# Performance work log

Measured on AMD Instinct MI355X. Metric: run time of the kernel, lower is better.

## Reference

```python
import jax, jax.numpy as jnp
import numpy as np

B, T, C = 2, 1024, 2048
H, N = 32, 64
D_DECAY = 96; D_AAA = 96; D_MV = 64; D_GATE = 256
EPS_GN = 1e-5 * 64.0  # eps * head_size_divisor**2, divisor=8


def setup_inputs() -> dict:
    key = jax.random.key(0)
    ks = jax.random.split(key, 24)
    rn = lambda k, s, sc=1.0: jax.random.normal(k, s, jnp.float32) * sc
    ru = lambda k, s: jax.random.uniform(k, s, jnp.float32)
    sw = C ** -0.5
    return dict(
        x=rn(ks[0], (B, T, C)),
        v_first=rn(ks[1], (B, T, C)),
        shift_state=rn(ks[2], (B, C)),
        wkv_state=jnp.zeros((B, H, N, N), jnp.float32),
        x_r=ru(ks[3], (1, 1, C)), x_w=ru(ks[4], (1, 1, C)), x_k=ru(ks[5], (1, 1, C)),
        x_v=ru(ks[6], (1, 1, C)), x_a=ru(ks[7], (1, 1, C)), x_g=ru(ks[8], (1, 1, C)),
        w0=jnp.linspace(-7.0, -2.0, C, dtype=jnp.float32).reshape(1, 1, C) + 0.5,
        w1=rn(ks[9], (C, D_DECAY), sw), w2=rn(ks[10], (D_DECAY, C), 0.1 * D_DECAY ** -0.5),
        a0=jnp.zeros((1, 1, C), jnp.float32),
        a1=rn(ks[11], (C, D_AAA), sw), a2=rn(ks[12], (D_AAA, C), 0.1 * D_AAA ** -0.5),
        v0=jnp.ones((1, 1, C), jnp.float32),
        v1=rn(ks[13], (C, D_MV), sw), v2=rn(ks[14], (D_MV, C), 0.1 * D_MV ** -0.5),
        g1=rn(ks[15], (C, D_GATE), sw), g2=rn(ks[16], (D_GATE, C), 0.1 * D_GATE ** -0.5),
        k_k=0.85 * jnp.ones((1, 1, C), jnp.float32),
        k_a=jnp.ones((1, 1, C), jnp.float32),
        r_k=rn(ks[17], (H, N), 0.1),
        W_r=rn(ks[18], (C, C), sw), W_k=rn(ks[19], (C, C), sw),
        W_v=rn(ks[20], (C, C), sw), W_o=rn(ks[21], (C, C), sw),
        gn_w=jnp.ones((C,), jnp.float32), gn_b=jnp.zeros((C,), jnp.float32),
    )


def _forward(x, v_first, shift_state, wkv_state, x_r, x_w, x_k, x_v, x_a, x_g,
             w0, w1, w2, a0, a1, a2, v0, v1, v2, g1, g2, k_k, k_a, r_k,
             W_r, W_k, W_v, W_o, gn_w, gn_b):
    # token shift (ZeroPad2d((0,0,1,-1)) == prepend shift_state, drop last)
    xx = jnp.concatenate([shift_state[:, None, :], x[:, :-1]], axis=1) - x
    xr = x + xx * x_r; xw = x + xx * x_w; xk = x + xx * x_k
    xv = x + xx * x_v; xa = x + xx * x_a; xg = x + xx * x_g
    r = xr @ W_r.T
    w = -jax.nn.softplus(-(w0 + jnp.tanh(xw @ w1) @ w2)) - 0.5  # <= -0.5
    k = xk @ W_k.T
    v = xv @ W_v.T
    v = v + (v_first - v) * jax.nn.sigmoid(v0 + (xv @ v1) @ v2)  # layer_id != 0
    a = jax.nn.sigmoid(a0 + (xa @ a1) @ a2)
    g = jax.nn.sigmoid(xg @ g1) @ g2
    kk = (k * k_k).reshape(B, T, H, N)
    kk = kk / jnp.maximum(jnp.linalg.norm(kk, axis=-1, keepdims=True), 1e-12)  # F.normalize
    k = k * (1.0 + (a - 1.0) * k_a)
    # RWKV-7 recurrence: S_t = S * diag(exp(-exp(w))) + (S a) b^T + v k^T ; o_t = S r
    wdec = jnp.exp(-jnp.exp(w))                           # [B,T,C] in (0,1)
    tm = lambda z: z.reshape(B, T, H, N).transpose(1, 0, 2, 3)  # -> [T,B,H,N]
    xs = (tm(r), tm(wdec), tm(k), tm(v),
          -kk.transpose(1, 0, 2, 3),
          (kk * a.reshape(B, T, H, N)).transpose(1, 0, 2, 3))

    def step(S, ins):  # S: [B,H,N_v,N_k]
        rr, ww, kc, vv, aa, bb = ins
        Sa = jnp.einsum('bhvk,bhk->bhv', S, aa)
        S = S * ww[:, :, None, :] + Sa[..., None] * bb[:, :, None, :] + vv[..., None] * kc[:, :, None, :]
        return S, jnp.einsum('bhvk,bhk->bhv', S, rr)

    S_f, o = jax.lax.scan(step, wkv_state, xs)
    o = o.transpose(1, 0, 2, 3)                           # [B,T,H,N]
    # GroupNorm(H, C): per-(B*T) sample, normalize each head's N channels
    mu = o.mean(-1, keepdims=True)
    var = o.var(-1, keepdims=True)
    o = (o - mu) * jax.lax.rsqrt(var + EPS_GN) * gn_w.reshape(H, N) + gn_b.reshape(H, N)
    rh = r.reshape(B, T, H, N); kh = k.reshape(B, T, H, N); vh = v.reshape(B, T, H, N)
    o = o + (rh * kh * r_k).sum(-1, keepdims=True) * vh
    out = (o.reshape(B, T, C) * g) @ W_o.T
    return out, S_f


def reference(x, v_first, shift_state, wkv_state, x_r, x_w, x_k, x_v, x_a, x_g,
              w0, w1, w2, a0, a1, a2, v0, v1, v2, g1, g2, k_k, k_a, r_k,
              W_r, W_k, W_v, W_o, gn_w, gn_b):
    out, S_f = _forward(x, v_first, shift_state, wkv_state, x_r, x_w, x_k, x_v, x_a, x_g,
                        w0, w1, w2, a0, a1, a2, v0, v1, v2, g1, g2, k_k, k_a, r_k,
                        W_r, W_k, W_v, W_o, gn_w, gn_b)
    return (out, S_f)
```

## Files before the change

kernel.cpp:

```cpp
#include <hip/hip_runtime.h>
#include <stdint.h>

typedef __attribute__((ext_vector_type(4))) float f32x4;
typedef __attribute__((ext_vector_type(8))) __bf16 bf16x8;

#define DEVINL __device__ __forceinline__

constexpr int T_LEN = 1024;
constexpr int CDIM  = 2048;
constexpr int MROWS = 2048;
constexpr size_t MC = (size_t)MROWS * CDIM;

constexpr size_t SZ_BF  = MC * 2;
constexpr size_t SZ_F32 = MC * 4;
constexpr size_t oXr  = 0;
constexpr size_t oXw  = oXr + SZ_BF;
constexpr size_t oXk  = oXw + SZ_BF;
constexpr size_t oXv  = oXk + SZ_BF;
constexpr size_t oXa  = oXv + SZ_BF;
constexpr size_t oXg  = oXa + SZ_BF;
constexpr size_t oWr  = oXg + SZ_BF;
constexpr size_t oWk  = oWr + SZ_BF;
constexpr size_t oWv  = oWk + SZ_BF;
constexpr size_t oWo  = oWv + SZ_BF;
constexpr size_t oW1T = oWo + SZ_BF;
constexpr size_t oA1T = oW1T + 524288;
constexpr size_t oV1T = oA1T + 524288;
constexpr size_t oG1T = oV1T + 524288;
constexpr size_t oW2T = oG1T + 1048576;
constexpr size_t oA2T = oW2T + 524288;
constexpr size_t oV2T = oA2T + 524288;
constexpr size_t oG2T = oV2T + 524288;
constexpr size_t oHw  = oG2T + 1048576;
constexpr size_t oHa  = oHw + 524288;
constexpr size_t oHv  = oHa + 524288;
constexpr size_t oHg  = oHv + 524288;
constexpr size_t oR   = oHg + 1048576;
constexpr size_t oK   = oR  + SZ_F32;
constexpr size_t oV   = oK  + SZ_F32;
constexpr size_t oWW  = oV  + SZ_F32;
constexpr size_t oAA  = oWW + SZ_F32;
constexpr size_t oBB  = oAA + SZ_F32;
constexpr size_t oG   = oBB + SZ_F32;
constexpr size_t oO   = oG  + SZ_F32;
constexpr size_t oAout= oO  + SZ_F32;

DEVINL unsigned short f2bf(float f) {
  uint32_t u = __builtin_bit_cast(uint32_t, f);
  u += 0x7fffu + ((u >> 16) & 1u);
  return (unsigned short)(u >> 16);
}
DEVINL void st_bf4(unsigned short* p, f32x4 v) {
  ushort4 o;
  o.x = f2bf(v[0]); o.y = f2bf(v[1]); o.z = f2bf(v[2]); o.w = f2bf(v[3]);
  *(ushort4*)p = o;
}
DEVINL void gload16(const void* g, void* l) {
  __builtin_amdgcn_global_load_lds(
      (const __attribute__((address_space(1))) unsigned int*)g,
      (__attribute__((address_space(3))) unsigned int*)l, 16, 0, 0);
}

DEVINL float red8(float x) {
  int y = __builtin_amdgcn_update_dpp(0, __builtin_bit_cast(int, x),
                                      0x128, 0xF, 0xF, true);
  return x + __builtin_bit_cast(float, y);
}
#if __has_builtin(__builtin_amdgcn_permlane16_swap)
DEVINL float red16(float x, bool evenrow) {
  unsigned xi = __builtin_bit_cast(unsigned, x);
  auto r = __builtin_amdgcn_permlane16_swap(xi, xi, false, false);
  unsigned oth = evenrow ? (unsigned)r[1] : (unsigned)r[0];
  return x + __builtin_bit_cast(float, oth);
}
#else
DEVINL float red16(float x, bool) { return x + __shfl_xor(x, 16); }
#endif
#if __has_builtin(__builtin_amdgcn_permlane32_swap)
DEVINL float red32(float x, bool lowhalf) {
  unsigned xi = __builtin_bit_cast(unsigned, x);
  auto r = __builtin_amdgcn_permlane32_swap(xi, xi, false, false);
  unsigned oth = lowhalf ? (unsigned)r[1] : (unsigned)r[0];
  return x + __builtin_bit_cast(float, oth);
}
#else
DEVINL float red32(float x, bool) { return x + __shfl_xor(x, 32); }
#endif

struct Conv4 { const float* s0; const float* s1; const float* s2; const float* s3;
               unsigned short* d0; unsigned short* d1; unsigned short* d2; unsigned short* d3; };
__global__ void k_conv4(Conv4 c, int n4) {
  int i = blockIdx.x * 256 + threadIdx.x;
  if (i >= n4) return;
  const float* s = (blockIdx.y == 0) ? c.s0 : (blockIdx.y == 1) ? c.s1
                   : (blockIdx.y == 2) ? c.s2 : c.s3;
  unsigned short* d = (blockIdx.y == 0) ? c.d0 : (blockIdx.y == 1) ? c.d1
                      : (blockIdx.y == 2) ? c.d2 : c.d3;
  f32x4 v = *(const f32x4*)(s + (size_t)i * 4);
  st_bf4(d + (size_t)i * 4, v);
}

struct TpJobs {
  const float* src[8];
  unsigned short* dst[8];
  int sR[8]; int sC[8]; int dR[8]; int dC[8];
};
__global__ void k_tp8(TpJobs jt) {
  const int j = blockIdx.y;
  const int n = jt.dR[j] * jt.dC[j];
  int i = blockIdx.x * 256 + threadIdx.x;
  if (i >= n) return;
  const int dC = jt.dC[j], sR = jt.sR[j], sC = jt.sC[j];
  int r = i / dC, c = i - r * dC;
  float v = (r < sC && c < sR) ? jt.src[j][(size_t)c * sC + r] : 0.f;
  jt.dst[j][i] = f2bf(v);
}

__global__ void k_mix(const float* __restrict__ x, const float* __restrict__ shift,
                      const float* __restrict__ cr, const float* __restrict__ cw,
                      const float* __restrict__ ck, const float* __restrict__ cv,
                      const float* __restrict__ ca, const float* __restrict__ cg,
                      unsigned short* __restrict__ Xr, unsigned short* __restrict__ Xw,
                      unsigned short* __restrict__ Xk, unsigned short* __restrict__ Xv,
                      unsigned short* __restrict__ Xa, unsigned short* __restrict__ Xg) {
  int i = blockIdx.x * 256 + threadIdx.x;
  size_t e = (size_t)i * 4;
  int m = (int)(e >> 11);
  int c = (int)(e & 2047);
  int t = m & (T_LEN - 1);
  int b = m >> 10;
  f32x4 xc = *(const f32x4*)(x + e);
  f32x4 pv = (t == 0) ? *(const f32x4*)(shift + (size_t)b * CDIM + c)
                      : *(const f32x4*)(x + e - CDIM);
  f32x4 xx = pv - xc;
  st_bf4(Xr + e, xc + xx * (*(const f32x4*)(cr + c)));
  st_bf4(Xw + e, xc + xx * (*(const f32x4*)(cw + c)));
  st_bf4(Xk + e, xc + xx * (*(const f32x4*)(ck + c)));
  st_bf4(Xv + e, xc + xx * (*(const f32x4*)(cv + c)));
  st_bf4(Xa + e, xc + xx * (*(const f32x4*)(ca + c)));
  st_bf4(Xg + e, xc + xx * (*(const f32x4*)(cg + c)));
}

struct GemmJob { const unsigned short* A; const unsigned short* B; void* C; int epi; int ldc; int n; };
struct GemmBatch { GemmJob j[4]; };

__global__ __launch_bounds__(256) void k_gemm_nt(GemmBatch gb, int K) {
  const GemmJob jb = gb.j[blockIdx.z];
  const int colB = blockIdx.x * 128;
  if (colB >= jb.n) return;
  const int ldc = jb.ldc;
  __shared__ __align__(16) unsigned short As[128 * 32];
  __shared__ __align__(16) unsigned short Bs[128 * 32];
  const int tid  = threadIdx.x;
  const int lane = tid & 63;
  const int wv   = tid >> 6;
  const int wm = wv >> 1, wn = wv & 1;
  const int rowB = blockIdx.y * 128;
  const size_t rsb = (size_t)K * 2;
  const int c0 = wv, c1 = wv + 4;
  const char* Ag0 = (const char*)jb.A + (size_t)(rowB + c0 * 16 + (lane >> 2)) * rsb + (lane & 3) * 16;
  const char* Ag1 = (const char*)jb.A + (size_t)(rowB + c1 * 16 + (lane >> 2)) * rsb + (lane & 3) * 16;
  const char* Bg0 = (const char*)jb.B + (size_t)(colB + c0 * 16 + (lane >> 2)) * rsb + (lane & 3) * 16;
  const char* Bg1 = (const char*)jb.B + (size_t)(colB + c1 * 16 + (lane >> 2)) * rsb + (lane & 3) * 16;
  unsigned short* Al0 = As + c0 * 512;
  unsigned short* Al1 = As + c1 * 512;
  unsigned short* Bl0 = Bs + c0 * 512;
  unsigned short* Bl1 = Bs + c1 * 512;
  f32x4 acc[4][4];
#pragma unroll
  for (int mi = 0; mi < 4; ++mi)
#pragma unroll
    for (int ni = 0; ni < 4; ++ni) acc[mi][ni] = (f32x4){0.f, 0.f, 0.f, 0.f};
  const int KT = K >> 5;
  const int fr = lane & 15, fk = (lane >> 4) * 8;
  for (int kt = 0; kt < KT; ++kt) {
    __syncthreads();
    gload16(Ag0, Al0); gload16(Ag1, Al1);
    gload16(Bg0, Bl0); gload16(Bg1, Bl1);
    Ag0 += 64; Ag1 += 64; Bg0 += 64; Bg1 += 64;
    __syncthreads();
    bf16x8 af[4], bfv[4];
#pragma unroll
    for (int mi = 0; mi < 4; ++mi)
      af[mi] = *(const bf16x8*)&As[(wm * 64 + mi * 16 + fr) * 32 + fk];
#pragma unroll
    for (int ni = 0; ni < 4; ++ni)
      bfv[ni] = *(const bf16x8*)&Bs[(wn * 64 + ni * 16 + fr) * 32 + fk];
#pragma unroll
    for (int mi = 0; mi < 4; ++mi)
#pragma unroll
      for (int ni = 0; ni < 4; ++ni)
        acc[mi][ni] = __builtin_amdgcn_mfma_f32_16x16x32_bf16(af[mi], bfv[ni], acc[mi][ni], 0, 0, 0);
  }
  const int er = (lane >> 4) * 4, ec = lane & 15;
  if (jb.epi == 0) {
    float* Cf = (float*)jb.C;
#pragma unroll
    for (int mi = 0; mi < 4; ++mi)
#pragma unroll
      for (int ni = 0; ni < 4; ++ni) {
        int row0 = rowB + wm * 64 + mi * 16 + er;
        int col  = colB + wn * 64 + ni * 16 + ec;
#pragma unroll
        for (int j = 0; j < 4; ++j)
          Cf[(size_t)(row0 + j) * ldc + col] = acc[mi][ni][j];
      }
  } else {
    unsigned short* Cb = (unsigned short*)jb.C;
#pragma unroll
    for (int mi = 0; mi < 4; ++mi)
#pragma unroll
      for (int ni = 0; ni < 4; ++ni) {
        int row0 = rowB + wm * 64 + mi * 16 + er;
        int col  = colB + wn * 64 + ni * 16 + ec;
#pragma unroll
        for (int j = 0; j < 4; ++j) {
          float val = acc[mi][ni][j];
          if (jb.epi == 2) val = tanhf(val);
          else if (jb.epi == 3) val = 1.f / (1.f + __expf(-val));
          Cb[(size_t)(row0 + j) * ldc + col] = f2bf(val);
        }
      }
  }
}

__global__ __launch_bounds__(256) void k_post(
    float* __restrict__ Kb, float* __restrict__ Vb, float* __restrict__ Wb,
    float* __restrict__ Ab, float* __restrict__ Bb,
    const float* __restrict__ vf, const float* __restrict__ w0,
    const float* __restrict__ a0, const float* __restrict__ v0,
    const float* __restrict__ kkc, const float* __restrict__ kac) {
  int gw = blockIdx.x * 4 + (threadIdx.x >> 6);
  int lane = threadIdx.x & 63;
  int m = gw >> 5, h = gw & 31;
  int c = h * 64 + lane;
  size_t idx = (size_t)m * CDIM + c;
  float kraw = Kb[idx], vraw = Vb[idx], wlr = Wb[idx], alr = Ab[idx], vlr = Bb[idx];
  float z = w0[c] + wlr;
  float sg = 1.f / (1.f + __expf(-z));
  float wdec = __expf(-0.60653065971f * sg);
  float a = 1.f / (1.f + __expf(-(a0[c] + alr)));
  float vgate = 1.f / (1.f + __expf(-(v0[c] + vlr)));
  float v = vraw + (vf[idx] - vraw) * vgate;
  float kk = kraw * kkc[c];
  float s2 = kk * kk;
#pragma unroll
  for (int off = 32; off; off >>= 1) s2 += __shfl_xor(s2, off);
  float inv = 1.f / fmaxf(sqrtf(s2), 1e-12f);
  kk *= inv;
  float kn = kraw * (1.f + (a - 1.f) * kac[c]);
  Wb[idx] = wdec; Vb[idx] = v; Kb[idx] = kn; Ab[idx] = -kk; Bb[idx] = kk * a;
}

__global__ __launch_bounds__(64) void k_scan(
    const float* __restrict__ Rb, const float* __restrict__ Wb,
    const float* __restrict__ Kb, const float* __restrict__ Vb,
    const float* __restrict__ Ab, const float* __restrict__ Bb,
    const float* __restrict__ S0, float* __restrict__ Ob,
    float* __restrict__ Sf) {
  const int bid = blockIdx.x;
  const int bh = bid & 63, vo = bid >> 6;
  const int b = bh >> 5, h = bh & 31;
  const int lane = threadIdx.x;
  const int vr = lane & 7;
  const int kq = lane >> 3;
  const int gv = vo * 8 + vr;
  const int kk0 = kq * 8;
  const bool evr = ((lane >> 4) & 1) == 0;
  const bool lhf = lane < 32;
  __shared__ __align__(16) float stg[4][6][64];
  const size_t rowBase = (size_t)b * T_LEN * CDIM;
  const size_t colBase = (size_t)h * 64;
  const float* pR = Rb + rowBase + colBase + lane;
  const float* pW = Wb + rowBase + colBase + lane;
  const float* pK = Kb + rowBase + colBase + lane;
  const float* pV = Vb + rowBase + colBase + lane;
  const float* pA = Ab + rowBase + colBase + lane;
  const float* pB = Bb + rowBase + colBase + lane;
  float* Obp = Ob + rowBase + colBase + vo * 8 + lane;
  f32x4 s0, s1;
  {
    const float* sp = S0 + (((size_t)(b * 32 + h)) * 64 + gv) * 64 + kk0;
    s0 = *(const f32x4*)sp; s1 = *(const f32x4*)(sp + 4);
  }
  float gA[6], gB[6];
  {
    float h0[6], h1[6];
    h0[0] = pR[0]; h0[1] = pW[0]; h0[2] = pK[0]; h0[3] = pV[0]; h0[4] = pA[0]; h0[5] = pB[0];
    h1[0] = pR[CDIM]; h1[1] = pW[CDIM]; h1[2] = pK[CDIM]; h1[3] = pV[CDIM]; h1[4] = pA[CDIM]; h1[5] = pB[CDIM];
#pragma unroll
    for (int j = 0; j < 6; ++j) { stg[0][j][lane] = h0[j]; stg[1][j][lane] = h1[j]; }
    gA[0] = pR[2 * CDIM]; gA[1] = pW[2 * CDIM]; gA[2] = pK[2 * CDIM];
    gA[3] = pV[2 * CDIM]; gA[4] = pA[2 * CDIM]; gA[5] = pB[2 * CDIM];
    gB[0] = pR[3 * CDIM]; gB[1] = pW[3 * CDIM]; gB[2] = pK[3 * CDIM];
    gB[3] = pV[3 * CDIM]; gB[4] = pA[3 * CDIM]; gB[5] = pB[3 * CDIM];
  }
  f32x4 aR0, aR1, aW0, aW1, aK0, aK1, aA0, aA1, aB0, aB1; float aVV;
  f32x4 bR0, bR1, bW0, bW1, bK0, bK1, bA0, bA1, bB0, bB1; float bVV;
  aR0 = *(const f32x4*)&stg[0][0][kk0]; aR1 = *(const f32x4*)&stg[0][0][kk0 + 4];
  aW0 = *(const f32x4*)&stg[0][1][kk0]; aW1 = *(const f32x4*)&stg[0][1][kk0 + 4];
  aK0 = *(const f32x4*)&stg[0][2][kk0]; aK1 = *(const f32x4*)&stg[0][2][kk0 + 4];
  aA0 = *(const f32x4*)&stg[0][4][kk0]; aA1 = *(const f32x4*)&stg[0][4][kk0 + 4];
  aB0 = *(const f32x4*)&stg[0][5][kk0]; aB1 = *(const f32x4*)&stg[0][5][kk0 + 4];
  aVV = stg[0][3][gv];
  float pox = 0.f;
#define SCAN_STEP(T, G, SR0,SR1,SW0,SW1,SK0,SK1,SA0,SA1,SB0,SB1,SVV,           \
                  NR0,NR1,NW0,NW1,NK0,NK1,NA0,NA1,NB0,NB1,NVV, FIRST) do {     \
    f32x4 _sv = SA0 * s0 + SA1 * s1;                                           \
    float _sa = _sv[0] + _sv[1] + _sv[2] + _sv[3];                             \
    { const int _np = ((T) + 1) & 3;          \
      NR0 = *(const f32x4*)&stg[_np][0][kk0]; NR1 = *(const f32x4*)&stg[_np][0][kk0 + 4]; \
      NW0 = *(const f32x4*)&stg[_np][1][kk0]; NW1 = *(const f32x4*)&stg[_np][1][kk0 + 4]; \
      NK0 = *(const f32x4*)&stg[_np][2][kk0]; NK1 = *(const f32x4*)&stg[_np][2][kk0 + 4]; \
      NA0 = *(const f32x4*)&stg[_np][4][kk0]; NA1 = *(const f32x4*)&stg[_np][4][kk0 + 4]; \
      NB0 = *(const f32x4*)&stg[_np][5][kk0]; NB1 = *(const f32x4*)&stg[_np][5][kk0 + 4]; \
      NVV = stg[_np][3][gv]; }                                                 \
    float _po = pox;                                                           \
    _sa = red8(_sa);        _po = red8(_po);                                   \
    _sa = red16(_sa, evr);  _po = red16(_po, evr);                             \
    _sa = red32(_sa, lhf);  _po = red32(_po, lhf);                             \
    if (!(FIRST) && lane < 8) Obp[(size_t)((T) - 1) * CDIM] = _po;             \
    { const int _ws = ((T) + 2) & 3;                                           \
      stg[_ws][0][lane] = G[0]; stg[_ws][1][lane] = G[1];                      \
      stg[_ws][2][lane] = G[2]; stg[_ws][3][lane] = G[3];                      \
      stg[_ws][4][lane] = G[4]; stg[_ws][5][lane] = G[5];                      \
      const size_t _to = (size_t)(((T) + 4 < T_LEN) ? (T) + 4 : T_LEN - 1) * CDIM; \
      G[0] = pR[_to]; G[1] = pW[_to]; G[2] = pK[_to];                          \
      G[3] = pV[_to]; G[4] = pA[_to]; G[5] = pB[_to]; }                        \
    s0 = s0 * SW0 + _sa * SB0 + SVV * SK0;                                     \
    s1 = s1 * SW1 + _sa * SB1 + SVV * SK1;                                     \
    f32x4 _ov = s0 * SR0 + s1 * SR1;                                           \
    pox = _ov[0] + _ov[1] + _ov[2] + _ov[3];                                   \
  } while (0)
#define SCAN_STEP_I(...) SCAN_STEP(__VA_ARGS__)
#define ASET aR0,aR1,aW0,aW1,aK0,aK1,aA0,aA1,aB0,aB1,aVV
#define BSET bR0,bR1,bW0,bW1,bK0,bK1,bA0,bA1,bB0,bB1,bVV
  SCAN_STEP_I(0, gA, ASET, BSET, true);
  SCAN_STEP_I(1, gB, BSET, ASET, false);
  for (int t = 2; t < T_LEN; t += 2) {
    SCAN_STEP_I(t, gA, ASET, BSET, false);
    SCAN_STEP_I(t + 1, gB, BSET, ASET, false);
  }
#undef SCAN_STEP
#undef SCAN_STEP_I
#undef ASET
#undef BSET
  {
    float _po = pox;
    _po = red8(_po);
    _po = red16(_po, evr);
    _po = red32(_po, lhf);
    if (lane < 8) Obp[(size_t)(T_LEN - 1) * CDIM] = _po;
  }
  float* sfp = Sf + (((size_t)(b * 32 + h)) * 64 + gv) * 64 + kk0;
  *(f32x4*)sfp = s0; *(f32x4*)(sfp + 4) = s1;
}

__global__ __launch_bounds__(256) void k_gn(
    const float* __restrict__ Ob, const float* __restrict__ Rb,
    const float* __restrict__ Kb, const float* __restrict__ Vb,
    const float* __restrict__ Gb, const float* __restrict__ rk,
    const float* __restrict__ gw, const float* __restrict__ gb2,
    unsigned short* __restrict__ Aout) {
  int gwv = blockIdx.x * 4 + (threadIdx.x >> 6);
  int lane = threadIdx.x & 63;
  int m = gwv >> 5, h = gwv & 31;
  int c = h * 64 + lane;
  size_t idx = (size_t)m * CDIM + c;
  float o = Ob[idx], r = Rb[idx], k = Kb[idx], v = Vb[idx], g = Gb[idx];
  float t1 = o, t2 = o * o, t3 = r * k * rk[c];
#pragma unroll
  for (int off = 32; off; off >>= 1) {
    t1 += __shfl_xor(t1, off);
    t2 += __shfl_xor(t2, off);
    t3 += __shfl_xor(t3, off);
  }
  float mean = t1 * (1.f / 64.f);
  float var = t2 * (1.f / 64.f) - mean * mean;
  float og = (o - mean) * rsqrtf(var + 6.4e-4f) * gw[c] + gb2[c];
  og += t3 * v;
  Aout[idx] = f2bf(og * g);
}

extern "C" void kernel_launch(void* const* d_in, const int* in_sizes, int n_in,
                              void* d_out, int out_size, void* d_ws, size_t ws_size,
                              hipStream_t stream) {
  (void)in_sizes; (void)n_in; (void)out_size; (void)ws_size;
  const float* x      = (const float*)d_in[0];
  const float* vfirst = (const float*)d_in[1];
  const float* shift  = (const float*)d_in[2];
  const float* wkv0   = (const float*)d_in[3];
  const float* xr_c   = (const float*)d_in[4];
  const float* xw_c   = (const float*)d_in[5];
  const float* xk_c   = (const float*)d_in[6];
  const float* xv_c   = (const float*)d_in[7];
  const float* xa_c   = (const float*)d_in[8];
  const float* xg_c   = (const float*)d_in[9];
  const float* w0     = (const float*)d_in[10];
  const float* w1     = (const float*)d_in[11];
  const float* w2     = (const float*)d_in[12];
  const float* a0     = (const float*)d_in[13];
  const float* a1     = (const float*)d_in[14];
  const float* a2     = (const float*)d_in[15];
  const float* v0     = (const float*)d_in[16];
  const float* v1     = (const float*)d_in[17];
  const float* v2     = (const float*)d_in[18];
  const float* g1     = (const float*)d_in[19];
  const float* g2     = (const float*)d_in[20];
  const float* k_k    = (const float*)d_in[21];
  const float* k_a    = (const float*)d_in[22];
  const float* r_k    = (const float*)d_in[23];
  const float* W_r    = (const float*)d_in[24];
  const float* W_k    = (const float*)d_in[25];
  const float* W_v    = (const float*)d_in[26];
  const float* W_o    = (const float*)d_in[27];
  const float* gn_w   = (const float*)d_in[28];
  const float* gn_b   = (const float*)d_in[29];
  char* ws = (char*)d_ws;
  auto BF = [&](size_t o) { return (unsigned short*)(ws + o); };
  auto FP = [&](size_t o) { return (float*)(ws + o); };

  { Conv4 cb{W_r, W_k, W_v, W_o, BF(oWr), BF(oWk), BF(oWv), BF(oWo)};
    k_conv4<<<dim3(4096, 4), 256, 0, stream>>>(cb, 1048576); }
  { TpJobs jt{};
    jt.src[0] = w1; jt.dst[0] = BF(oW1T); jt.sR[0] = 2048; jt.sC[0] = 96;   jt.dR[0] = 128;  jt.dC[0] = 2048;
    jt.src[1] = a1; jt.dst[1] = BF(oA1T); jt.sR[1] = 2048; jt.sC[1] = 96;   jt.dR[1] = 128;  jt.dC[1] = 2048;
    jt.src[2] = v1; jt.dst[2] = BF(oV1T); jt.sR[2] = 2048; jt.sC[2] = 64;   jt.dR[2] = 128;  jt.dC[2] = 2048;
    jt.src[3] = g1; jt.dst[3] = BF(oG1T); jt.sR[3] = 2048; jt.sC[3] = 256;  jt.dR[3] = 256;  jt.dC[3] = 2048;
    jt.src[4] = w2; jt.dst[4] = BF(oW2T); jt.sR[4] = 96;   jt.sC[4] = 2048; jt.dR[4] = 2048; jt.dC[4] = 128;
    jt.src[5] = a2; jt.dst[5] = BF(oA2T); jt.sR[5] = 96;   jt.sC[5] = 2048; jt.dR[5] = 2048; jt.dC[5] = 128;
    jt.src[6] = v2; jt.dst[6] = BF(oV2T); jt.sR[6] = 64;   jt.sC[6] = 2048; jt.dR[6] = 2048; jt.dC[6] = 128;
    jt.src[7] = g2; jt.dst[7] = BF(oG2T); jt.sR[7] = 256;  jt.sC[7] = 2048; jt.dR[7] = 2048; jt.dC[7] = 256;
    k_tp8<<<dim3(2048, 8), 256, 0, stream>>>(jt); }
  k_mix<<<4096, 256, 0, stream>>>(x, shift, xr_c, xw_c, xk_c, xv_c, xa_c, xg_c,
                                  BF(oXr), BF(oXw), BF(oXk), BF(oXv), BF(oXa), BF(oXg));
  { GemmBatch gb{};
    gb.j[0] = {BF(oXr), BF(oWr), FP(oR), 0, 2048, 2048};
    gb.j[1] = {BF(oXk), BF(oWk), FP(oK), 0, 2048, 2048};
    gb.j[2] = {BF(oXv), BF(oWv), FP(oV), 0, 2048, 2048};
    k_gemm_nt<<<dim3(16, 16, 3), 256, 0, stream>>>(gb, 2048); }
  { GemmBatch gb{};
    gb.j[0] = {BF(oXw), BF(oW1T), BF(oHw), 2, 128, 128};
    gb.j[1] = {BF(oXa), BF(oA1T), BF(oHa), 1, 128, 128};
    gb.j[2] = {BF(oXv), BF(oV1T), BF(oHv), 1, 128, 128};
    gb.j[3] = {BF(oXg), BF(oG1T), BF(oHg), 3, 256, 256};
    k_gemm_nt<<<dim3(2, 16, 4), 256, 0, stream>>>(gb, 2048); }
  { GemmBatch gb{};
    gb.j[0] = {BF(oHw), BF(oW2T), FP(oWW), 0, 2048, 2048};
    gb.j[1] = {BF(oHa), BF(oA2T), FP(oAA), 0, 2048, 2048};
    gb.j[2] = {BF(oHv), BF(oV2T), FP(oBB), 0, 2048, 2048};
    k_gemm_nt<<<dim3(16, 16, 3), 256, 0, stream>>>(gb, 128); }
  { GemmBatch gb{};
    gb.j[0] = {BF(oHg), BF(oG2T), FP(oG), 0, 2048, 2048};
    k_gemm_nt<<<dim3(16, 16, 1), 256, 0, stream>>>(gb, 256); }
  k_post<<<16384, 256, 0, stream>>>(FP(oK), FP(oV), FP(oWW), FP(oAA), FP(oBB),
                                    vfirst, w0, a0, v0, k_k, k_a);
  k_scan<<<512, 64, 0, stream>>>(FP(oR), FP(oWW), FP(oK), FP(oV), FP(oAA), FP(oBB),
                                 wkv0, FP(oO), (float*)d_out + MC);
  k_gn<<<16384, 256, 0, stream>>>(FP(oO), FP(oR), FP(oK), FP(oV), FP(oG),
                                  r_k, gn_w, gn_b, BF(oAout));
  { GemmBatch gb{};
    gb.j[0] = {BF(oAout), BF(oWo), d_out, 0, 2048, 2048};
    k_gemm_nt<<<dim3(16, 16, 1), 256, 0, stream>>>(gb, 2048); }
}
```

Measured before the change: 587.1 us.

## Halve per-wave state rows in WKV scan and double scan grid

The recurrent scan kernel now gives each wave 4 value rows instead of 8, with each lane holding 4 state elements instead of 8. The grid doubles from 512 to 1024 single-wave blocks, so there are more independent waves per CU to hide the latency of the sequential per-step dependency chain. In exchange, every block still loads the full per-step r/w/k/v/a/b vectors, so global and LDS staging traffic doubles. The cross-lane reduction also gains an extra DPP rotate step, which lengthens each step's critical path.

```diff
diff --git a/kernel.cpp b/kernel.cpp
--- a/kernel.cpp
+++ b/kernel.cpp
@@ -61,9 +61,10 @@
       (__attribute__((address_space(3))) unsigned int*)l, 16, 0, 0);
 }
 
-DEVINL float red8(float x) {
+template <int CTL>
+DEVINL float redrot(float x) {
   int y = __builtin_amdgcn_update_dpp(0, __builtin_bit_cast(int, x),
-                                      0x128, 0xF, 0xF, true);
+                                      CTL, 0xF, 0xF, true);
   return x + __builtin_bit_cast(float, y);
 }
 #if __has_builtin(__builtin_amdgcn_permlane16_swap)
@@ -262,10 +263,10 @@
   const int bh = bid & 63, vo = bid >> 6;
   const int b = bh >> 5, h = bh & 31;
   const int lane = threadIdx.x;
-  const int vr = lane & 7;
-  const int kq = lane >> 3;
-  const int gv = vo * 8 + vr;
-  const int kk0 = kq * 8;
+  const int vr = lane & 3;
+  const int kq = lane >> 2;
+  const int gv = vo * 4 + vr;
+  const int kk0 = kq * 4;
   const bool evr = ((lane >> 4) & 1) == 0;
   const bool lhf = lane < 32;
   __shared__ __align__(16) float stg[4][6][64];
@@ -277,11 +278,11 @@
   const float* pV = Vb + rowBase + colBase + lane;
   const float* pA = Ab + rowBase + colBase + lane;
   const float* pB = Bb + rowBase + colBase + lane;
-  float* Obp = Ob + rowBase + colBase + vo * 8 + lane;
-  f32x4 s0, s1;
+  float* Obp = Ob + rowBase + colBase + vo * 4 + lane;
+  f32x4 s0;
   {
     const float* sp = S0 + (((size_t)(b * 32 + h)) * 64 + gv) * 64 + kk0;
-    s0 = *(const f32x4*)sp; s1 = *(const f32x4*)(sp + 4);
+    s0 = *(const f32x4*)sp;
   }
   float gA[6], gB[6];
   {
@@ -295,31 +296,31 @@
     gB[0] = pR[3 * CDIM]; gB[1] = pW[3 * CDIM]; gB[2] = pK[3 * CDIM];
     gB[3] = pV[3 * CDIM]; gB[4] = pA[3 * CDIM]; gB[5] = pB[3 * CDIM];
   }
-  f32x4 aR0, aR1, aW0, aW1, aK0, aK1, aA0, aA1, aB0, aB1; float aVV;
-  f32x4 bR0, bR1, bW0, bW1, bK0, bK1, bA0, bA1, bB0, bB1; float bVV;
-  aR0 = *(const f32x4*)&stg[0][0][kk0]; aR1 = *(const f32x4*)&stg[0][0][kk0 + 4];
-  aW0 = *(const f32x4*)&stg[0][1][kk0]; aW1 = *(const f32x4*)&stg[0][1][kk0 + 4];
-  aK0 = *(const f32x4*)&stg[0][2][kk0]; aK1 = *(const f32x4*)&stg[0][2][kk0 + 4];
-  aA0 = *(const f32x4*)&stg[0][4][kk0]; aA1 = *(const f32x4*)&stg[0][4][kk0 + 4];
-  aB0 = *(const f32x4*)&stg[0][5][kk0]; aB1 = *(const f32x4*)&stg[0][5][kk0 + 4];
+  f32x4 aR, aW, aK, aA, aB; float aVV;
+  f32x4 bR, bW, bK, bA, bB; float bVV;
+  aR = *(const f32x4*)&stg[0][0][kk0];
+  aW = *(const f32x4*)&stg[0][1][kk0];
+  aK = *(const f32x4*)&stg[0][2][kk0];
+  aA = *(const f32x4*)&stg[0][4][kk0];
+  aB = *(const f32x4*)&stg[0][5][kk0];
   aVV = stg[0][3][gv];
   float pox = 0.f;
-#define SCAN_STEP(T, G, SR0,SR1,SW0,SW1,SK0,SK1,SA0,SA1,SB0,SB1,SVV,           \
-                  NR0,NR1,NW0,NW1,NK0,NK1,NA0,NA1,NB0,NB1,NVV, FIRST) do {     \
-    f32x4 _sv = SA0 * s0 + SA1 * s1;                                           \
+#define SCAN_STEP(T, G, SR,SW,SK,SA,SB,SVV, NR,NW,NK,NA,NB,NVV, FIRST) do {    \
+    f32x4 _sv = SA * s0;                                                       \
     float _sa = _sv[0] + _sv[1] + _sv[2] + _sv[3];                             \
     { const int _np = ((T) + 1) & 3;          \
-      NR0 = *(const f32x4*)&stg[_np][0][kk0]; NR1 = *(const f32x4*)&stg[_np][0][kk0 + 4]; \
-      NW0 = *(const f32x4*)&stg[_np][1][kk0]; NW1 = *(const f32x4*)&stg[_np][1][kk0 + 4]; \
-      NK0 = *(const f32x4*)&stg[_np][2][kk0]; NK1 = *(const f32x4*)&stg[_np][2][kk0 + 4]; \
-      NA0 = *(const f32x4*)&stg[_np][4][kk0]; NA1 = *(const f32x4*)&stg[_np][4][kk0 + 4]; \
-      NB0 = *(const f32x4*)&stg[_np][5][kk0]; NB1 = *(const f32x4*)&stg[_np][5][kk0 + 4]; \
+      NR = *(const f32x4*)&stg[_np][0][kk0];                                   \
+      NW = *(const f32x4*)&stg[_np][1][kk0];                                   \
+      NK = *(const f32x4*)&stg[_np][2][kk0];                                   \
+      NA = *(const f32x4*)&stg[_np][4][kk0];                                   \
+      NB = *(const f32x4*)&stg[_np][5][kk0];                                   \
       NVV = stg[_np][3][gv]; }                                                 \
     float _po = pox;                                                           \
-    _sa = red8(_sa);        _po = red8(_po);                                   \
-    _sa = red16(_sa, evr);  _po = red16(_po, evr);                             \
-    _sa = red32(_sa, lhf);  _po = red32(_po, lhf);                             \
-    if (!(FIRST) && lane < 8) Obp[(size_t)((T) - 1) * CDIM] = _po;             \
+    _sa = redrot<0x124>(_sa); _po = redrot<0x124>(_po);                        \
+    _sa = redrot<0x128>(_sa); _po = redrot<0x128>(_po);                        \
+    _sa = red16(_sa, evr);    _po = red16(_po, evr);                           \
+    _sa = red32(_sa, lhf);    _po = red32(_po, lhf);                           \
+    if (!(FIRST) && lane < 4) Obp[(size_t)((T) - 1) * CDIM] = _po;             \
     { const int _ws = ((T) + 2) & 3;                                           \
       stg[_ws][0][lane] = G[0]; stg[_ws][1][lane] = G[1];                      \
       stg[_ws][2][lane] = G[2]; stg[_ws][3][lane] = G[3];                      \
@@ -327,14 +328,13 @@
       const size_t _to = (size_t)(((T) + 4 < T_LEN) ? (T) + 4 : T_LEN - 1) * CDIM; \
       G[0] = pR[_to]; G[1] = pW[_to]; G[2] = pK[_to];                          \
       G[3] = pV[_to]; G[4] = pA[_to]; G[5] = pB[_to]; }                        \
-    s0 = s0 * SW0 + _sa * SB0 + SVV * SK0;                                     \
-    s1 = s1 * SW1 + _sa * SB1 + SVV * SK1;                                     \
-    f32x4 _ov = s0 * SR0 + s1 * SR1;                                           \
+    s0 = s0 * SW + _sa * SB + SVV * SK;                                        \
+    f32x4 _ov = s0 * SR;                                                       \
     pox = _ov[0] + _ov[1] + _ov[2] + _ov[3];                                   \
   } while (0)
 #define SCAN_STEP_I(...) SCAN_STEP(__VA_ARGS__)
-#define ASET aR0,aR1,aW0,aW1,aK0,aK1,aA0,aA1,aB0,aB1,aVV
-#define BSET bR0,bR1,bW0,bW1,bK0,bK1,bA0,bA1,bB0,bB1,bVV
+#define ASET aR,aW,aK,aA,aB,aVV
+#define BSET bR,bW,bK,bA,bB,bVV
   SCAN_STEP_I(0, gA, ASET, BSET, true);
   SCAN_STEP_I(1, gB, BSET, ASET, false);
   for (int t = 2; t < T_LEN; t += 2) {
@@ -347,13 +347,14 @@
 #undef BSET
   {
     float _po = pox;
-    _po = red8(_po);
+    _po = redrot<0x124>(_po);
+    _po = redrot<0x128>(_po);
     _po = red16(_po, evr);
     _po = red32(_po, lhf);
-    if (lane < 8) Obp[(size_t)(T_LEN - 1) * CDIM] = _po;
+    if (lane < 4) Obp[(size_t)(T_LEN - 1) * CDIM] = _po;
   }
   float* sfp = Sf + (((size_t)(b * 32 + h)) * 64 + gv) * 64 + kk0;
-  *(f32x4*)sfp = s0; *(f32x4*)(sfp + 4) = s1;
+  *(f32x4*)sfp = s0;
 }
 
 __global__ __launch_bounds__(256) void k_gn(
@@ -455,8 +456,8 @@
     k_gemm_nt<<<dim3(16, 16, 1), 256, 0, stream>>>(gb, 256); }
   k_post<<<16384, 256, 0, stream>>>(FP(oK), FP(oV), FP(oWW), FP(oAA), FP(oBB),
                                     vfirst, w0, a0, v0, k_k, k_a);
-  k_scan<<<512, 64, 0, stream>>>(FP(oR), FP(oWW), FP(oK), FP(oV), FP(oAA), FP(oBB),
-                                 wkv0, FP(oO), (float*)d_out + MC);
+  k_scan<<<1024, 64, 0, stream>>>(FP(oR), FP(oWW), FP(oK), FP(oV), FP(oAA), FP(oBB),
+                                  wkv0, FP(oO), (float*)d_out + MC);
   k_gn<<<16384, 256, 0, stream>>>(FP(oO), FP(oR), FP(oK), FP(oV), FP(oG),
                                   r_k, gn_w, gn_b, BF(oAout));
   { GemmBatch gb{};
```

Measured after the change: 593.3 us. Within noise of the previous version (+1.1%).
